# Performance work log

Hardware: AMD Instinct MI355X
Metric: run time of the kernel (lower is better)

The kernel has to match this reference:

```python
import jax, jax.numpy as jnp
import numpy as np

SCALE_XY = 0.1
SCALE_WH = 0.2
CRITERIA = 0.5        # NMS IoU threshold
MAX_OUTPUT = 100      # max detections per image
SCORE_THRESH = 0.05   # pre-NMS score threshold
MIN_SIZE = 1.0 / 300.0  # min box width/height
TOP_K = 400           # fixed-size candidate set for jit-compatible NMS


def setup_inputs() -> dict:
    key = jax.random.key(0)
    k1, k2, k3, k4 = jax.random.split(key, 4)
    N, C, B = 32, 81, 8732
    bboxes_in = jax.random.normal(k1, (N, 4, B), jnp.float32)
    scores_in = jax.random.normal(k2, (N, C, B), jnp.float32)
    # synthetic but realistic default boxes: centers in [0,1], wh in [0.02,0.4]
    xy = jax.random.uniform(k3, (B, 2), jnp.float32)
    wh = jax.random.uniform(k4, (B, 2), jnp.float32, minval=0.02, maxval=0.4)
    dboxes_xywh = jnp.concatenate([xy, wh], axis=-1)[None]  # [1, B, 4]
    return {"bboxes_in": bboxes_in, "scores_in": scores_in, "dboxes_xywh": dboxes_xywh}


def _scale_back(bboxes_in, scores_in, dboxes):
    # bboxes_in [N,4,B] -> [N,B,4]; scores_in [N,C,B] -> [N,B,C]
    bb = jnp.transpose(bboxes_in, (0, 2, 1))
    sc = jnp.transpose(scores_in, (0, 2, 1))
    xy = SCALE_XY * bb[..., :2] * dboxes[..., 2:] + dboxes[..., :2]
    wh = jnp.exp(SCALE_WH * bb[..., 2:]) * dboxes[..., 2:]
    ltrb = jnp.concatenate([xy - 0.5 * wh, xy + 0.5 * wh], axis=-1)  # [N,B,4]
    probs = jax.nn.softmax(sc, axis=-1)                               # [N,B,C]
    return ltrb, probs


def _decode_single(boxes, probs):
    # boxes [B,4] (ltrb), probs [B,C]
    B, C = probs.shape
    boxes = jnp.clip(boxes, 0.0, 1.0)
    sc = probs[:, 1:]  # drop background class 0 -> [B, C-1]
    w = boxes[:, 2] - boxes[:, 0]
    h = boxes[:, 3] - boxes[:, 1]
    valid_box = (w >= MIN_SIZE) & (h >= MIN_SIZE)
    valid = (sc > SCORE_THRESH) & valid_box[:, None]
    flat = jnp.where(valid, sc, -1.0).reshape(-1)  # [B*(C-1)], row-major: box then class
    vals, idx = jax.lax.top_k(flat, TOP_K)         # sorted desc by score
    box_idx = idx // (C - 1)
    labels = idx % (C - 1) + 1                     # class ids 1..C-1
    cboxes = boxes[box_idx]                        # [K,4]
    cscores = sc.reshape(-1)[idx]                  # [K] (differentiable gather)
    kvalid = vals > 0.0
    # batched_nms trick: offset boxes by label so different classes never overlap
    off = labels.astype(boxes.dtype)[:, None] * 2.0  # coords are in [0,1]
    ob = cboxes + off
    lt = jnp.maximum(ob[:, None, :2], ob[None, :, :2])
    rb = jnp.minimum(ob[:, None, 2:], ob[None, :, 2:])
    inter = jnp.prod(jnp.clip(rb - lt, 0.0, None), axis=-1)         # [K,K]
    area = jnp.prod(jnp.clip(ob[:, 2:] - ob[:, :2], 0.0, None), axis=-1)
    iou = inter / jnp.maximum(area[:, None] + area[None, :] - inter, 1e-12)
    order = jnp.arange(TOP_K)

    def body(i, keep):
        sup = keep[i] & (iou[i] > CRITERIA) & (order > i)
        return keep & ~sup

    keep = jax.lax.fori_loop(0, TOP_K, body, kvalid)
    final = jnp.where(keep, cscores, -1.0)
    out_s, out_i = jax.lax.top_k(final, MAX_OUTPUT)  # first MAX_OUTPUT kept, score order
    ok = out_s > 0.0
    out_boxes = jnp.where(ok[:, None], cboxes[out_i], 0.0)
    out_labels = jnp.where(ok, labels[out_i], 0)
    out_scores = jnp.where(ok, cscores[out_i], 0.0)
    return out_boxes, out_labels, out_scores


def reference(bboxes_in, scores_in, dboxes_xywh):
    ltrb, probs = _scale_back(bboxes_in, scores_in, dboxes_xywh)
    boxes, labels, scores = jax.vmap(_decode_single)(ltrb, probs)
    return boxes, labels, scores  # [N,100,4], [N,100] int, [N,100]
```

## Files before the change

kernel.cpp:

```cpp
#include <hip/hip_runtime.h>
#include <cstdint>
#include <cstddef>

#define NIMG 32
#define NCLS 81
#define NC1  80
#define NBOX 8732
#define CAP  65536
#define TOPK 400
#define MAXOUT 100
#define KW   7
#define COLCAP 2048
#define BDEC 256
#define CNTSTRIDE 16
#define RSTRIDE 409

__device__ __forceinline__ unsigned int f2sort(float f) {
    unsigned int u = __float_as_uint(f);
    return (u & 0x80000000u) ? ~u : (u | 0x80000000u);
}

__global__ __launch_bounds__(BDEC) void k_decode(const float* __restrict__ bboxes,
        const float* __restrict__ scores, const float* __restrict__ dbox,
        float4* __restrict__ oboxes, uint2* __restrict__ cand, int* __restrict__ cnt) {
    int n = blockIdx.y;
    int b = blockIdx.x * BDEC + threadIdx.x;
    int lane = threadIdx.x & 63;
    bool live = (b < NBOX);
    int bs = live ? b : 0;

    const float* sp = scores + (size_t)n * NCLS * NBOX + bs;
    float sc[NCLS];
    #pragma unroll
    for (int c = 0; c < NCLS; ++c) sc[c] = sp[(size_t)c * NBOX];

    bool go = false;
    float l = 0.f, tt = 0.f, r = 0.f, bo = 0.f;
    if (live) {
        const float* bp = bboxes + (size_t)n * 4 * NBOX + b;
        float bx = bp[0], by = bp[NBOX], bw = bp[2 * NBOX], bh = bp[3 * NBOX];
        float4 d = reinterpret_cast<const float4*>(dbox)[b];
        float cx = 0.1f * bx * d.z + d.x;
        float cy = 0.1f * by * d.w + d.y;
        float ww = expf(0.2f * bw) * d.z;
        float hh = expf(0.2f * bh) * d.w;
        l = cx - 0.5f * ww;  tt = cy - 0.5f * hh;
        r = cx + 0.5f * ww;  bo = cy + 0.5f * hh;
        l = fminf(fmaxf(l, 0.f), 1.f);  tt = fminf(fmaxf(tt, 0.f), 1.f);
        r = fminf(fmaxf(r, 0.f), 1.f);  bo = fminf(fmaxf(bo, 0.f), 1.f);
        const float MINS = 1.0f / 300.0f;
        go = (r - l >= MINS) && (bo - tt >= MINS);
    }

    float m = -3.4e38f;
    #pragma unroll
    for (int c = 0; c < NCLS; ++c) m = fmaxf(m, sc[c]);

    float ss = 0.f;
    #pragma unroll
    for (int c = 0; c < NCLS; ++c) { sc[c] = expf(sc[c] - m); ss += sc[c]; }

    unsigned long long mlo = 0ull;
    unsigned int       mhi = 0u;
    #pragma unroll
    for (int c = 1; c < NCLS; ++c) {
        float p = sc[c] / ss;
        sc[c] = p;
        if (go && (p > 0.05f)) {
            if (c <= 64) mlo |= 1ull << (c - 1);
            else         mhi |= 1u << (c - 65);
        }
    }

    int nc = (int)__popcll(mlo) + __popc(mhi);
    int incl = nc;
    #pragma unroll
    for (int off = 1; off < 64; off <<= 1) {
        int u = __shfl_up(incl, off);
        if (lane >= off) incl += u;
    }
    int excl = incl - nc;
    int tot = __shfl(incl, 63);
    int base = 0;
    if (lane == 0 && tot > 0) base = atomicAdd(&cnt[n * CNTSTRIDE], tot);
    base = __shfl(base, 0);

    if (nc > 0) {
        int pos = base + excl;
        uint2* cp = cand + (size_t)n * CAP;
        #pragma unroll
        for (int c = 1; c < NCLS; ++c) {
            bool bit = (c <= 64) ? (((mlo >> (c - 1)) & 1ull) != 0)
                                 : (((mhi >> (c - 65)) & 1u) != 0);
            if (bit) {
                if (pos < CAP) cp[pos] = make_uint2(__float_as_uint(sc[c]),
                                                    (unsigned)(b * NC1 + (c - 1)));
                ++pos;
            }
        }
    }

    if (live && nc > 0) oboxes[(size_t)n * NBOX + b] = make_float4(l, tt, r, bo);
}

__device__ void bitonic_desc(unsigned long long* arr, int nn, int tid, int nt) {
    for (int k = 2; k <= nn; k <<= 1) {
        for (int j = k >> 1; j > 0; j >>= 1) {
            __syncthreads();
            for (int i = tid; i < nn; i += nt) {
                int ixj = i ^ j;
                if (ixj > i) {
                    unsigned long long a = arr[i], b = arr[ixj];
                    bool desc = ((i & k) == 0);
                    bool sw = desc ? (a < b) : (a > b);
                    if (sw) { arr[i] = b; arr[ixj] = a; }
                }
            }
        }
    }
    __syncthreads();
}

__global__ __launch_bounds__(1024) void k_topk(const float4* __restrict__ boxes,
        const uint2* __restrict__ cand, const int* __restrict__ cnt,
        float* __restrict__ g_sc, float4* __restrict__ g_cb, int* __restrict__ g_lab,
        float4* __restrict__ g_ob, float* __restrict__ g_ar, int* __restrict__ g_nsel) {
    __shared__ int hist[1024];
    __shared__ unsigned long long keys[COLCAP];
    __shared__ int s_T, s_pos;

    int n = blockIdx.x;
    int tid = threadIdx.x;
    int lane = tid & 63;
    unsigned long long lmlt = (1ull << lane) - 1ull;
    int M = cnt[n * CNTSTRIDE]; if (M > CAP) M = CAP;
    const uint2* cp = cand + (size_t)n * CAP;

    hist[tid] = 0;
    if (tid == 0) s_pos = 0;
    __syncthreads();

    for (int i = tid; i < M; i += 1024) {
        unsigned int bits = cp[i].x;
        int bk = (int)(bits >> 16) - 0x3D00;
        bk = max(0, min(1023, bk));
        atomicAdd(&hist[bk], 1);
    }
    __syncthreads();

    if (tid < 64) {
        int sl = 0;
        #pragma unroll
        for (int t = 0; t < 16; ++t) sl += hist[tid * 16 + t];
        int incl = sl;
        #pragma unroll
        for (int off = 1; off < 64; off <<= 1) {
            int v = __shfl_down(incl, off);
            if (tid + off < 64) incl += v;
        }
        int xl = incl - sl;
        int tc = -1, cum = xl;
        for (int t = 15; t >= 0; --t) {
            cum += hist[tid * 16 + t];
            if (cum >= TOPK) { tc = tid * 16 + t; break; }
        }
        #pragma unroll
        for (int off = 32; off > 0; off >>= 1)
            tc = max(tc, __shfl_xor(tc, off));
        if (tid == 0) s_T = max(tc, 0);
    }
    __syncthreads();
    int T = s_T;

    int iters = (M + 1023) / 1024;
    for (int it = 0; it < iters; ++it) {
        int i = it * 1024 + tid;
        bool pred = false; unsigned long long key = 0ull;
        if (i < M) {
            uint2 e = cp[i];
            int bk = (int)(e.x >> 16) - 0x3D00;
            bk = max(0, min(1023, bk));
            if (bk >= T) {
                pred = true;
                key = ((unsigned long long)e.x << 32) | (unsigned int)(~e.y);
            }
        }
        unsigned long long mask = __ballot(pred);
        int base = 0;
        if (lane == 0) {
            int cw = (int)__popcll(mask);
            if (cw) base = atomicAdd(&s_pos, cw);
        }
        base = __shfl(base, 0);
        if (pred) {
            int pos = base + (int)__popcll(mask & lmlt);
            if (pos < COLCAP) keys[pos] = key;
        }
    }
    __syncthreads();
    int ncol = min(s_pos, COLCAP);

    int nsort = 512;
    while (nsort < ncol) nsort <<= 1;
    for (int i = ncol + tid; i < nsort; i += 1024) keys[i] = 0ull;
    __syncthreads();
    bitonic_desc(keys, nsort, tid, 1024);

    int nsel = min(TOPK, ncol);
    if (tid < TOPK) {
        int i = tid;
        float sc = -1.0f; float4 cb = make_float4(0.f, 0.f, 0.f, 0.f);
        int lab = 0; float4 ob = cb; float ar = 0.f;
        if (i < nsel) {
            unsigned long long key = keys[i];
            unsigned int bits = (unsigned int)(key >> 32);
            unsigned int flat = ~(unsigned int)key;
            int bb = (int)(flat / NC1);
            lab = (int)(flat - (unsigned)bb * NC1) + 1;
            sc = __uint_as_float(bits);
            cb = boxes[(size_t)n * NBOX + bb];
            float off = 2.0f * (float)lab;
            ob = make_float4(cb.x + off, cb.y + off, cb.z + off, cb.w + off);
            ar = fmaxf(ob.z - ob.x, 0.f) * fmaxf(ob.w - ob.y, 0.f);
        }
        size_t gi = (size_t)n * TOPK + i;
        g_sc[gi] = sc; g_cb[gi] = cb; g_lab[gi] = lab; g_ob[gi] = ob; g_ar[gi] = ar;
    }
    if (tid == 0) g_nsel[n] = nsel;
}

__global__ __launch_bounds__(256) void k_iou(const float4* __restrict__ g_ob,
        const float* __restrict__ g_ar, const int* __restrict__ g_nsel,
        unsigned long long* __restrict__ g_rows) {
    __shared__ float4 s_ob[TOPK];
    __shared__ float  s_ar[TOPK];
    int n = blockIdx.y, w = blockIdx.x;
    int tid = threadIdx.x;
    for (int i = tid; i < TOPK; i += 256) {
        s_ob[i] = g_ob[(size_t)n * TOPK + i];
        s_ar[i] = g_ar[(size_t)n * TOPK + i];
    }
    __syncthreads();
    int nsel = g_nsel[n];
    int j0 = w * 64;
    unsigned long long* gr = g_rows + ((size_t)n * KW + w) * TOPK;
    for (int i = tid; i < TOPK; i += 256) {
        unsigned long long cur = 0ull;
        if (i < nsel) {
            float4 oi = s_ob[i]; float ai = s_ar[i];
            int jend = min(j0 + 64, nsel);
            for (int j = j0; j < jend; ++j) {
                if (j > i) {
                    float4 oj = s_ob[j];
                    float lx = fmaxf(oi.x, oj.x), ly = fmaxf(oi.y, oj.y);
                    float rx = fminf(oi.z, oj.z), ry = fminf(oi.w, oj.w);
                    float inter = fmaxf(rx - lx, 0.f) * fmaxf(ry - ly, 0.f);
                    float uni = fmaxf(ai + s_ar[j] - inter, 1e-12f);
                    cur |= ((unsigned long long)(inter / uni > 0.5f)) << (j - j0);
                }
            }
        }
        gr[i] = cur;
    }
}

__global__ __launch_bounds__(512) void k_nms(const unsigned long long* __restrict__ g_rows,
        const float* __restrict__ g_sc, const float4* __restrict__ g_cb,
        const int* __restrict__ g_lab, const int* __restrict__ g_nsel,
        float* __restrict__ out) {
    __shared__ unsigned long long rows[KW * RSTRIDE];
    __shared__ unsigned long long nz[8];
    __shared__ unsigned long long s_keep[KW];
    __shared__ int pc[KW + 1];

    int n = blockIdx.x;
    int tid = threadIdx.x;
    int lane = tid & 63;
    int nsel = g_nsel[n];

    const unsigned long long* gr = g_rows + (size_t)n * KW * TOPK;
    for (int t = tid; t < KW * TOPK; t += 512) {
        int w = t / TOPK, i = t - w * TOPK;
        rows[w * RSTRIDE + i] = gr[t];
    }
    __syncthreads();

    {
        unsigned long long v = 0ull;
        if (tid < TOPK) {
            #pragma unroll
            for (int w = 0; w < KW; ++w) v |= rows[w * RSTRIDE + tid];
        }
        unsigned long long bal = __ballot(v != 0ull);
        if (lane == 0) nz[tid >> 6] = bal;
    }
    __syncthreads();

    if (tid < 64) {
        unsigned long long keepw = 0ull;
        if (lane < KW) {
            int lo = lane << 6;
            keepw = (nsel >= lo + 64) ? ~0ull
                  : (nsel <= lo ? 0ull : ((1ull << (nsel - lo)) - 1ull));
        }
        #pragma unroll
        for (int w = 0; w < KW; ++w) {
            unsigned long long nzw = nz[w];
            while (nzw) {
                int bq = (int)__ffsll((long long)nzw) - 1;
                nzw &= nzw - 1;
                int i = (w << 6) + bq;
                unsigned long long row = (lane < KW) ? rows[lane * RSTRIDE + i] : 0ull;
                unsigned long long kwv = __shfl(keepw, w);
                if ((kwv >> bq) & 1ull) keepw &= ~row;
            }
        }
        if (lane < KW) s_keep[lane] = keepw;
    }
    __syncthreads();

    if (tid == 0) {
        int acc = 0;
        #pragma unroll
        for (int w = 0; w < KW; ++w) { pc[w] = acc; acc += (int)__popcll(s_keep[w]); }
        pc[KW] = acc;
    }
    __syncthreads();

    float* obox = out;
    float* olab = out + (size_t)NIMG * MAXOUT * 4;
    float* osco = out + (size_t)NIMG * MAXOUT * 5;
    int nkept = pc[KW];

    if (tid < TOPK) {
        unsigned long long kw = s_keep[tid >> 6];
        bool kb = (kw >> (tid & 63)) & 1ull;
        if (kb) {
            int rank = pc[tid >> 6] + (int)__popcll(kw & ((1ull << (tid & 63)) - 1ull));
            if (rank < MAXOUT) {
                size_t gi = (size_t)n * TOPK + tid;
                float4 cb = g_cb[gi];
                size_t bo_ = ((size_t)n * MAXOUT + rank) * 4;
                obox[bo_ + 0] = cb.x; obox[bo_ + 1] = cb.y;
                obox[bo_ + 2] = cb.z; obox[bo_ + 3] = cb.w;
                olab[(size_t)n * MAXOUT + rank] = (float)g_lab[gi];
                osco[(size_t)n * MAXOUT + rank] = g_sc[gi];
            }
        }
    }
    if (tid < MAXOUT && tid >= nkept) {
        size_t bo_ = ((size_t)n * MAXOUT + tid) * 4;
        obox[bo_ + 0] = 0.f; obox[bo_ + 1] = 0.f; obox[bo_ + 2] = 0.f; obox[bo_ + 3] = 0.f;
        olab[(size_t)n * MAXOUT + tid] = 0.f;
        osco[(size_t)n * MAXOUT + tid] = 0.f;
    }
}

extern "C" void kernel_launch(void* const* d_in, const int* in_sizes, int n_in,
                              void* d_out, int out_size, void* d_ws, size_t ws_size,
                              hipStream_t stream) {
    (void)in_sizes; (void)n_in; (void)out_size; (void)ws_size;
    const float* bboxes = (const float*)d_in[0];
    const float* scores = (const float*)d_in[1];
    const float* dbox   = (const float*)d_in[2];
    float* out = (float*)d_out;

    char* ws = (char*)d_ws;
    size_t off = 0;
    float4* oboxes = (float4*)(ws + off); off += (size_t)NIMG * NBOX * sizeof(float4);
    int* cnt = (int*)(ws + off); off += (size_t)NIMG * CNTSTRIDE * sizeof(int);
    uint2* cand = (uint2*)(ws + off); off += (size_t)NIMG * CAP * sizeof(uint2);
    float* g_sc = (float*)(ws + off); off += (size_t)NIMG * TOPK * sizeof(float);
    float4* g_cb = (float4*)(ws + off); off += (size_t)NIMG * TOPK * sizeof(float4);
    int* g_lab = (int*)(ws + off); off += (size_t)NIMG * TOPK * sizeof(int);
    float4* g_ob = (float4*)(ws + off); off += (size_t)NIMG * TOPK * sizeof(float4);
    float* g_ar = (float*)(ws + off); off += (size_t)NIMG * TOPK * sizeof(float);
    int* g_nsel = (int*)(ws + off); off += 256;
    unsigned long long* g_rows = (unsigned long long*)(ws + off);
    off += (size_t)NIMG * KW * TOPK * sizeof(unsigned long long);

    hipMemsetAsync(cnt, 0, NIMG * CNTSTRIDE * sizeof(int), stream);

    int gx = (NBOX + BDEC - 1) / BDEC;
    k_decode<<<dim3(gx, NIMG), BDEC, 0, stream>>>(bboxes, scores, dbox, oboxes, cand, cnt);
    k_topk<<<NIMG, 1024, 0, stream>>>(oboxes, cand, cnt, g_sc, g_cb, g_lab, g_ob, g_ar, g_nsel);
    k_iou<<<dim3(KW, NIMG), 256, 0, stream>>>(g_ob, g_ar, g_nsel, g_rows);
    k_nms<<<NIMG, 512, 0, stream>>>(g_rows, g_sc, g_cb, g_lab, g_nsel, out);
}
```

Before: 109.2 us.

## Split decode softmax across two threads per box with thresholded mask

The decode kernel now assigns two threads per box, each loading and exponentiating about half of the 81 class scores (41 each, overlapping at class 40), which halves per-thread register arrays and doubles the thread count. The max and sum are combined with lane shuffles, and the per-class division is replaced by comparing exp values against 0.05*sum, falling back to an exact divide only near the threshold. Candidate probabilities are recomputed by reloading the score only for the selected classes. This aims to raise occupancy and memory-level parallelism in the bandwidth-heavy decode stage, at the cost of extra shuffles and redundant reloads for emitted candidates.

```diff
diff --git a/kernel.cpp b/kernel.cpp
--- a/kernel.cpp
+++ b/kernel.cpp
@@ -24,19 +24,23 @@
         const float* __restrict__ scores, const float* __restrict__ dbox,
         float4* __restrict__ oboxes, uint2* __restrict__ cand, int* __restrict__ cnt) {
     int n = blockIdx.y;
-    int b = blockIdx.x * BDEC + threadIdx.x;
-    int lane = threadIdx.x & 63;
+    int tid = threadIdx.x;
+    int lane = tid & 63;
+    int half = tid & 1;
+    int b = blockIdx.x * (BDEC / 2) + (tid >> 1);
     bool live = (b < NBOX);
-    int bs = live ? b : 0;
+    int bs = live ? b : (NBOX - 1);
 
     const float* sp = scores + (size_t)n * NCLS * NBOX + bs;
-    float sc[NCLS];
+    const float* spc = sp + (size_t)(half ? 40 : 0) * NBOX;
+
+    float e[41];
     #pragma unroll
-    for (int c = 0; c < NCLS; ++c) sc[c] = sp[(size_t)c * NBOX];
+    for (int i = 0; i < 41; ++i) e[i] = spc[(size_t)i * NBOX];
 
     bool go = false;
     float l = 0.f, tt = 0.f, r = 0.f, bo = 0.f;
-    if (live) {
+    if (live && !half) {
         const float* bp = bboxes + (size_t)n * 4 * NBOX + b;
         float bx = bp[0], by = bp[NBOX], bw = bp[2 * NBOX], bh = bp[3 * NBOX];
         float4 d = reinterpret_cast<const float4*>(dbox)[b];
@@ -52,27 +56,48 @@
         go = (r - l >= MINS) && (bo - tt >= MINS);
     }
 
-    float m = -3.4e38f;
+    float mh = -3.4e38f;
     #pragma unroll
-    for (int c = 0; c < NCLS; ++c) m = fmaxf(m, sc[c]);
-
-    float ss = 0.f;
+    for (int i = 0; i < 41; ++i) mh = fmaxf(mh, e[i]);
+    float m = fmaxf(mh, __shfl_xor(mh, 1));
+
     #pragma unroll
-    for (int c = 0; c < NCLS; ++c) { sc[c] = expf(sc[c] - m); ss += sc[c]; }
-
-    unsigned long long mlo = 0ull;
-    unsigned int       mhi = 0u;
+    for (int i = 0; i < 41; ++i) e[i] = expf(e[i] - m);
+
+    float acc = 0.f;
+    if (!half) {
+        #pragma unroll
+        for (int i = 0; i < 41; ++i) acc += e[i];
+    }
+    float pre = __shfl_xor(acc, 1);
+    float st = 0.f;
+    if (half) {
+        st = pre;
+        #pragma unroll
+        for (int i = 1; i < 41; ++i) st += e[i];
+    }
+    float so = __shfl_xor(st, 1);
+    float ss = half ? st : so;
+
+    int goi = go ? 1 : 0;
+    int gop = __shfl_xor(goi, 1);
+    bool goB = (half ? gop : goi) != 0;
+
+    float t05 = 0.05f * ss;
+    float thi = t05 * 1.000001f;
+    float tlo = t05 * 0.999999f;
+    unsigned long long msk = 0ull;
     #pragma unroll
-    for (int c = 1; c < NCLS; ++c) {
-        float p = sc[c] / ss;
-        sc[c] = p;
-        if (go && (p > 0.05f)) {
-            if (c <= 64) mlo |= 1ull << (c - 1);
-            else         mhi |= 1u << (c - 65);
-        }
-    }
-
-    int nc = (int)__popcll(mlo) + __popc(mhi);
+    for (int i = 1; i < 41; ++i) {
+        float ev = e[i];
+        bool bit;
+        if (ev > thi)       bit = true;
+        else if (ev < tlo)  bit = false;
+        else                bit = (ev / ss > 0.05f);
+        if (goB && bit) msk |= 1ull << i;
+    }
+
+    int nc = (int)__popcll(msk);
     int incl = nc;
     #pragma unroll
     for (int off = 1; off < 64; off <<= 1) {
@@ -85,22 +110,24 @@
     if (lane == 0 && tot > 0) base = atomicAdd(&cnt[n * CNTSTRIDE], tot);
     base = __shfl(base, 0);
 
+    int cbase = half ? 40 : 0;
     if (nc > 0) {
         int pos = base + excl;
         uint2* cp = cand + (size_t)n * CAP;
-        #pragma unroll
-        for (int c = 1; c < NCLS; ++c) {
-            bool bit = (c <= 64) ? (((mlo >> (c - 1)) & 1ull) != 0)
-                                 : (((mhi >> (c - 65)) & 1u) != 0);
-            if (bit) {
-                if (pos < CAP) cp[pos] = make_uint2(__float_as_uint(sc[c]),
-                                                    (unsigned)(b * NC1 + (c - 1)));
-                ++pos;
-            }
-        }
-    }
-
-    if (live && nc > 0) oboxes[(size_t)n * NBOX + b] = make_float4(l, tt, r, bo);
+        unsigned long long ml = msk;
+        while (ml) {
+            int i = (int)__ffsll((long long)ml) - 1; ml &= ml - 1;
+            int c = cbase + i;
+            float x = sp[(size_t)c * NBOX];
+            float p = expf(x - m) / ss;
+            if (pos < CAP) cp[pos] = make_uint2(__float_as_uint(p),
+                                                (unsigned)(b * NC1 + (c - 1)));
+            ++pos;
+        }
+    }
+
+    int pnc = nc + __shfl_xor(nc, 1);
+    if (live && !half && pnc > 0) oboxes[(size_t)n * NBOX + b] = make_float4(l, tt, r, bo);
 }
 
 __device__ void bitonic_desc(unsigned long long* arr, int nn, int tid, int nt) {
@@ -381,7 +408,7 @@
 
     hipMemsetAsync(cnt, 0, NIMG * CNTSTRIDE * sizeof(int), stream);
 
-    int gx = (NBOX + BDEC - 1) / BDEC;
+    int gx = (NBOX + (BDEC / 2) - 1) / (BDEC / 2);
     k_decode<<<dim3(gx, NIMG), BDEC, 0, stream>>>(bboxes, scores, dbox, oboxes, cand, cnt);
     k_topk<<<NIMG, 1024, 0, stream>>>(oboxes, cand, cnt, g_sc, g_cb, g_lab, g_ob, g_ar, g_nsel);
     k_iou<<<dim3(KW, NIMG), 256, 0, stream>>>(g_ob, g_ar, g_nsel, g_rows);
```

New measurement: 100.3 us. -8.2%, faster.
